# Kernel optimization log

Measured on AMD Instinct MI355X. Metric: run time of the kernel, lower is better.

Reference implementation:

```python
import jax, jax.numpy as jnp
import numpy as np

N = 4096       # num nodes == output_dim (delta is symmetrized NxN)
E = 65536      # num edges (avg degree 16)
IN_DIM = 128
H = 256        # hidden_dim (channels)
HEADS = 4


def setup_inputs():
    key = jax.random.key(0)
    ks = iter(jax.random.split(key, 40))
    def w(shape, s=0.05):
        return jax.random.normal(next(ks), shape, jnp.float32) * s
    inp = {}
    inp['x'] = jax.random.normal(next(ks), (N, IN_DIM), jnp.float32)
    inp['edge_index'] = jax.random.randint(next(ks), (2, E), 0, N)
    inp['pre_w'] = w((H, IN_DIM)); inp['pre_b'] = w((H,))
    for p in ('g1', 'g2'):
        inp[p + '_gcn_w'] = w((H, H)); inp[p + '_gcn_b'] = w((H,))
        inp[p + '_attn_in_w'] = w((3 * H, H)); inp[p + '_attn_in_b'] = w((3 * H,))
        inp[p + '_attn_out_w'] = w((H, H)); inp[p + '_attn_out_b'] = w((H,))
        inp[p + '_ffn_w1'] = w((2 * H, H)); inp[p + '_ffn_b1'] = w((2 * H,))
        inp[p + '_ffn_w2'] = w((H, 2 * H)); inp[p + '_ffn_b2'] = w((H,))
    inp['mlp_w1'] = w((H, H)); inp['mlp_b1'] = w((H,))
    inp['mlp_w2'] = w((N, H)); inp['mlp_b2'] = w((N,))
    return inp


def _gcn(x, src, dst, W, b):
    n = x.shape[0]
    x = x @ W.T
    loop = jnp.arange(n)
    s = jnp.concatenate([src, loop])
    d = jnp.concatenate([dst, loop])
    deg = jax.ops.segment_sum(jnp.ones(s.shape[0], x.dtype), d, num_segments=n)
    dinv = jnp.where(deg > 0, jax.lax.rsqrt(deg), 0.0)
    coef = (dinv[s] * dinv[d])[:, None]
    out = jax.ops.segment_sum(x[s] * coef, d, num_segments=n)
    return out + b


def _mha(h, in_w, in_b, out_w, out_b):
    # nn.MultiheadAttention self-attention over all N nodes (single dense graph)
    n, c = h.shape
    d = c // HEADS
    qkv = h @ in_w.T + in_b                      # [N, 3C]
    q, k, v = jnp.split(qkv, 3, axis=-1)
    q = q.reshape(n, HEADS, d).transpose(1, 0, 2) * (d ** -0.5)  # [h, n, d]
    k = k.reshape(n, HEADS, d).transpose(1, 0, 2)
    v = v.reshape(n, HEADS, d).transpose(1, 0, 2)
    a = jax.nn.softmax(jnp.einsum('hnd,hmd->hnm', q, k), axis=-1)
    o = jnp.einsum('hnm,hmd->hnd', a, v).transpose(1, 0, 2).reshape(n, c)
    return o @ out_w.T + out_b


def _gps(x, src, dst, gw, gb, iw, ib, ow, ob, w1, b1, w2, b2):
    # GPSConv, eval mode: dropout off, batch_norm (default running stats) = identity
    h1 = _gcn(x, src, dst, gw, gb) + x
    h2 = _mha(x, iw, ib, ow, ob) + x
    out = h1 + h2
    ff = jax.nn.relu(out @ w1.T + b1) @ w2.T + b2
    return out + ff


def reference(x, edge_index, pre_w, pre_b,
              g1_gcn_w, g1_gcn_b, g1_attn_in_w, g1_attn_in_b, g1_attn_out_w, g1_attn_out_b,
              g1_ffn_w1, g1_ffn_b1, g1_ffn_w2, g1_ffn_b2,
              g2_gcn_w, g2_gcn_b, g2_attn_in_w, g2_attn_in_b, g2_attn_out_w, g2_attn_out_b,
              g2_ffn_w1, g2_ffn_b1, g2_ffn_w2, g2_ffn_b2,
              mlp_w1, mlp_b1, mlp_w2, mlp_b2):
    src, dst = edge_index[0], edge_index[1]
    h = jax.nn.relu(x @ pre_w.T + pre_b)
    h = jax.nn.relu(_gps(h, src, dst, g1_gcn_w, g1_gcn_b, g1_attn_in_w, g1_attn_in_b,
                         g1_attn_out_w, g1_attn_out_b, g1_ffn_w1, g1_ffn_b1, g1_ffn_w2, g1_ffn_b2))
    h = jax.nn.relu(_gps(h, src, dst, g2_gcn_w, g2_gcn_b, g2_attn_in_w, g2_attn_in_b,
                         g2_attn_out_w, g2_attn_out_b, g2_ffn_w1, g2_ffn_b1, g2_ffn_w2, g2_ffn_b2))
    delta = jax.nn.relu(h @ mlp_w1.T + mlp_b1) @ mlp_w2.T + mlp_b2  # [N, N]
    return (delta + delta.T) * 0.5
```

## Files before the change

kernel.cpp:

```cpp
#include <hip/hip_runtime.h>

#define NN 4096
#define EE 65536
#define HC 256

typedef unsigned short ushort_t;
typedef __attribute__((ext_vector_type(8))) short bf16x8;
typedef __attribute__((ext_vector_type(4))) float f32x4;
typedef __attribute__((ext_vector_type(16))) float f32x16;

__device__ __forceinline__ ushort_t f2bf(float f) {
    unsigned int u = __float_as_uint(f);
    unsigned int r = (u + 0x7fffu + ((u >> 16) & 1u)) >> 16;
    return (ushort_t)r;
}
__device__ __forceinline__ float bf2f(ushort_t u) {
    return __uint_as_float(((unsigned int)u) << 16);
}
__device__ __forceinline__ unsigned int pack2bf(float a, float b) {
    unsigned int ua = __float_as_uint(a) + 0x8000u;
    unsigned int ub = __float_as_uint(b) + 0x8000u;
    return __builtin_amdgcn_perm(ub, ua, 0x07060302u);
}

__global__ void deg_init_k(float* __restrict__ deg) {
    int i = blockIdx.x * 256 + threadIdx.x;
    deg[i] = 1.0f;
}
__global__ void deg_scatter_k(const int* __restrict__ dst, float* __restrict__ deg) {
    int e = blockIdx.x * 256 + threadIdx.x;
    atomicAdd(&deg[dst[e]], 1.0f);
}
__global__ void dinv_k(const float* __restrict__ deg, float* __restrict__ dinv) {
    int i = blockIdx.x * 256 + threadIdx.x;
    dinv[i] = rsqrtf(deg[i]);
}
__global__ __launch_bounds__(1024)
void scan_offsets_k(const float* __restrict__ deg, int* __restrict__ offs,
                    int* __restrict__ cursor) {
    __shared__ int part[1024];
    const int t = threadIdx.x;
    int c0 = (int)deg[t * 4 + 0] - 1;
    int c1 = (int)deg[t * 4 + 1] - 1;
    int c2 = (int)deg[t * 4 + 2] - 1;
    int c3 = (int)deg[t * 4 + 3] - 1;
    part[t] = c0 + c1 + c2 + c3;
    __syncthreads();
    for (int off = 1; off < 1024; off <<= 1) {
        int v = (t >= off) ? part[t - off] : 0;
        __syncthreads();
        part[t] += v;
        __syncthreads();
    }
    int base = (t == 0) ? 0 : part[t - 1];
    offs[t * 4 + 0] = base;
    offs[t * 4 + 1] = base + c0;
    offs[t * 4 + 2] = base + c0 + c1;
    offs[t * 4 + 3] = base + c0 + c1 + c2;
    cursor[t * 4 + 0] = base;
    cursor[t * 4 + 1] = base + c0;
    cursor[t * 4 + 2] = base + c0 + c1;
    cursor[t * 4 + 3] = base + c0 + c1 + c2;
    if (t == 1023) offs[4096] = part[1023];
}
__global__ void csr_fill_k(const int* __restrict__ src, const int* __restrict__ dst,
                           int* __restrict__ cursor, int* __restrict__ csr_src) {
    int e = blockIdx.x * 256 + threadIdx.x;
    int pos = atomicAdd(&cursor[dst[e]], 1);
    csr_src[pos] = src[e];
}

__global__ __launch_bounds__(256)
void gcn_gather_k(const float* __restrict__ xw, const float* __restrict__ dinv,
                  const int* __restrict__ offs, const int* __restrict__ csr_src,
                  float* __restrict__ agg) {
    const int node = blockIdx.x * 4 + (threadIdx.x >> 6);
    const int c = (threadIdx.x & 63) * 4;
    const float dd = dinv[node];
    float4 a = *(const float4*)&xw[(size_t)node * HC + c];
    const float self = dd * dd;
    float4 acc = make_float4(a.x * self, a.y * self, a.z * self, a.w * self);
    const int beg = offs[node], end = offs[node + 1];
    for (int e = beg; e < end; e++) {
        int s = csr_src[e];
        float coef = dinv[s] * dd;
        const float4 v = *(const float4*)&xw[(size_t)s * HC + c];
        acc.x += v.x * coef;
        acc.y += v.y * coef;
        acc.z += v.z * coef;
        acc.w += v.w * coef;
    }
    *(float4*)&agg[(size_t)node * HC + c] = acc;
}

__global__ void cvt_bf16_k(const float* __restrict__ in, ushort_t* __restrict__ out) {
    int i = (blockIdx.x * 256 + threadIdx.x) * 4;
    float4 v = *(const float4*)&in[i];
    unsigned int d0 = pack2bf(v.x, v.y), d1 = pack2bf(v.z, v.w);
    *(uint2*)&out[i] = make_uint2(d0, d1);
}

__global__ __launch_bounds__(256)
void gemm_bf_k(const float* __restrict__ X, const float* __restrict__ W,
               const float* __restrict__ bias1, const float* __restrict__ bias2,
               const float* __restrict__ res1, const float* __restrict__ res2, float res2scale,
               float* __restrict__ out, int K, int M, int dorelu, int obf,
               int colsplit, const float* __restrict__ W2,
               const float* __restrict__ bias_r2, float* __restrict__ out2, int M2)
{
    __shared__ ushort_t As[64][72];
    __shared__ ushort_t Bs[32][72];
    const int t = threadIdx.x;
    const int w = t >> 6, lane = t & 63;
    const int m = lane & 15, quad = lane >> 4;
    const int row0 = blockIdx.y << 6, col0 = blockIdx.x << 5;
    const int sr = t >> 2;
    const int sc = (t & 3) << 4;
    const int wr2 = t >> 3;
    const int wc2 = (t & 7) << 3;

    const float* Wu = W;
    const float* b1u = bias1;
    const float* b2u = bias2;
    float* outu = out;
    int Mu = M, colu = col0;
    if (colsplit > 0 && col0 >= colsplit) {
        Wu = W2; b1u = bias_r2; b2u = nullptr;
        outu = out2; Mu = M2; colu = col0 - colsplit;
    }

    f32x4 acc[2] = {};
    for (int k0 = 0; k0 < K; k0 += 64) {
        const float* xp = &X[(size_t)(row0 + sr) * K + k0 + sc];
        const float* wp = &Wu[(size_t)(colu + wr2) * K + k0 + wc2];
        float4 xa = *(const float4*)xp,       xb = *(const float4*)(xp + 4);
        float4 xc = *(const float4*)(xp + 8), xd = *(const float4*)(xp + 12);
        float4 wa = *(const float4*)wp,       wb = *(const float4*)(wp + 4);
        __syncthreads();
        {
            unsigned int tx[8];
            tx[0] = pack2bf(xa.x, xa.y); tx[1] = pack2bf(xa.z, xa.w);
            tx[2] = pack2bf(xb.x, xb.y); tx[3] = pack2bf(xb.z, xb.w);
            tx[4] = pack2bf(xc.x, xc.y); tx[5] = pack2bf(xc.z, xc.w);
            tx[6] = pack2bf(xd.x, xd.y); tx[7] = pack2bf(xd.z, xd.w);
            *(uint4*)&As[sr][sc]     = *(const uint4*)&tx[0];
            *(uint4*)&As[sr][sc + 8] = *(const uint4*)&tx[4];
            unsigned int tw[4];
            tw[0] = pack2bf(wa.x, wa.y); tw[1] = pack2bf(wa.z, wa.w);
            tw[2] = pack2bf(wb.x, wb.y); tw[3] = pack2bf(wb.z, wb.w);
            *(uint4*)&Bs[wr2][wc2] = *(const uint4*)&tw[0];
        }
        __syncthreads();
        #pragma unroll
        for (int kc = 0; kc < 2; kc++) {
            bf16x8 af = *(const bf16x8*)&As[(w << 4) + m][kc * 32 + quad * 8];
            #pragma unroll
            for (int cb = 0; cb < 2; cb++) {
                bf16x8 bf = *(const bf16x8*)&Bs[cb * 16 + m][kc * 32 + quad * 8];
                acc[cb] = __builtin_amdgcn_mfma_f32_16x16x32_bf16(af, bf, acc[cb], 0, 0, 0);
            }
        }
    }
    #pragma unroll
    for (int cb = 0; cb < 2; cb++) {
        #pragma unroll
        for (int r = 0; r < 4; r++) {
            const int row = row0 + (w << 4) + quad * 4 + r;
            const int col = colu + cb * 16 + m;
            float v = acc[cb][r];
            if (b1u) v += b1u[col];
            if (b2u) v += b2u[col];
            if (res1) v += res1[(size_t)row * Mu + col];
            if (res2) v += res2scale * res2[(size_t)row * Mu + col];
            if (dorelu) v = fmaxf(v, 0.f);
            if (obf) ((ushort_t*)outu)[(size_t)row * Mu + col] = f2bf(v);
            else outu[(size_t)row * Mu + col] = v;
        }
    }
}

__global__ __launch_bounds__(256)
void kv_prep_k(const float* __restrict__ qkv, ushort_t* __restrict__ Kb,
               ushort_t* __restrict__ Vtb)
{
    __shared__ ushort_t Vs[64][72];
    const int h = blockIdx.y;
    const int n0 = blockIdx.x << 6;
    const int t = threadIdx.x;
    for (int u = t; u < 1024; u += 256) {
        int r = u >> 4, c = u & 15;
        const float* kp = &qkv[(size_t)(n0 + r) * 768 + 256 + h * 64 + c * 4];
        float4 kv = *(const float4*)kp;
        float4 vv = *(const float4*)(kp + 256);
        *(uint2*)&Kb[((size_t)(h * 4096 + n0 + r)) * 64 + c * 4] =
            make_uint2(pack2bf(kv.x, kv.y), pack2bf(kv.z, kv.w));
        *(uint2*)&Vs[r][c * 4] =
            make_uint2(pack2bf(vv.x, vv.y), pack2bf(vv.z, vv.w));
    }
    __syncthreads();
    int d = t >> 2, kc = t & 3;
    __attribute__((aligned(16))) ushort_t vals[16];
    #pragma unroll
    for (int k = 0; k < 16; k++) vals[k] = Vs[kc * 16 + k][d];
    ushort_t* op = &Vtb[((size_t)(h * 64 + d)) * 4096 + n0 + kc * 16];
    *(uint4*)op = *(const uint4*)&vals[0];
    *(uint4*)(op + 8) = *(const uint4*)&vals[8];
}

__global__ __launch_bounds__(128)
void attn_part_k(const float* qkv, const ushort_t* __restrict__ Kb,
                 const ushort_t* __restrict__ Vtb, ushort_t* opart,
                 float* __restrict__ m_part, float* __restrict__ l_part)
{
    __shared__ ushort_t Kt[64][64];
    __shared__ ushort_t Vt[64][64];
    const int h = blockIdx.y & 3;
    const int split = blockIdx.y >> 2;
    const int q0 = blockIdx.x << 6;
    const int t = threadIdx.x;
    const int w = t >> 6;
    const int lane = t & 63;
    const int l31 = lane & 31;
    const int hi = lane >> 5;

    const int sr = t >> 3;
    const int sc = t & 7;
    const int swz = ((sc ^ (sr & 7)) << 3);
    const ushort_t* kp = &Kb[((size_t)(h * 4096 + split * 1024 + sr)) * 64 + sc * 8];
    const ushort_t* vp = &Vtb[((size_t)(h * 64 + sr)) * 4096 + split * 1024 + sc * 8];

    const float qs = 0.125f * 1.44269504f;
    const int qrow = q0 + w * 32 + l31;
    bf16x8 qf[4];
    #pragma unroll
    for (int s = 0; s < 4; s++) {
        const float* qp = &qkv[(size_t)qrow * 768 + h * 64 + s * 16 + hi * 8];
        float4 a = *(const float4*)qp;
        float4 b = *(const float4*)(qp + 4);
        union { uint4 u; bf16x8 v; } cv;
        cv.u = make_uint4(pack2bf(a.x * qs, a.y * qs), pack2bf(a.z * qs, a.w * qs),
                          pack2bf(b.x * qs, b.y * qs), pack2bf(b.z * qs, b.w * qs));
        qf[s] = cv.v;
    }

    f32x16 O0 = {}, O1 = {};
    float mrow = -1e30f;
    float ol = 0.f;

    for (int it = 0; it < 16; it++) {
        uint4 k0 = *(const uint4*)kp;
        uint4 k1 = *(const uint4*)(kp + 16 * 64);
        uint4 k2 = *(const uint4*)(kp + 32 * 64);
        uint4 k3 = *(const uint4*)(kp + 48 * 64);
        uint4 v0 = *(const uint4*)vp;
        uint4 v1 = *(const uint4*)(vp + (size_t)16 * 4096);
        uint4 v2 = *(const uint4*)(vp + (size_t)32 * 4096);
        uint4 v3 = *(const uint4*)(vp + (size_t)48 * 4096);
        kp += 4096; vp += 64;
        __syncthreads();
        *(uint4*)&Kt[sr][swz]      = k0;
        *(uint4*)&Kt[sr + 16][swz] = k1;
        *(uint4*)&Kt[sr + 32][swz] = k2;
        *(uint4*)&Kt[sr + 48][swz] = k3;
        *(uint4*)&Vt[sr][swz]      = v0;
        *(uint4*)&Vt[sr + 16][swz] = v1;
        *(uint4*)&Vt[sr + 32][swz] = v2;
        *(uint4*)&Vt[sr + 48][swz] = v3;
        __syncthreads();

        f32x16 S0 = {}, S1 = {};
        const int kcol = ((hi) ^ (l31 & 7));
        (void)kcol;
        __builtin_amdgcn_s_setprio(1);
        #pragma unroll
        for (int s = 0; s < 4; s++) {
            const int cc = ((2 * s + hi) ^ (l31 & 7)) << 3;
            bf16x8 kf0 = *(const bf16x8*)&Kt[l31][cc];
            bf16x8 kf1 = *(const bf16x8*)&Kt[l31 + 32][cc];
            S0 = __builtin_amdgcn_mfma_f32_32x32x16_bf16(kf0, qf[s], S0, 0, 0, 0);
            S1 = __builtin_amdgcn_mfma_f32_32x32x16_bf16(kf1, qf[s], S1, 0, 0, 0);
        }
        __builtin_amdgcn_s_setprio(0);

        float r[32];
        #pragma unroll
        for (int i = 0; i < 16; i++) { r[i] = S0[i]; r[16 + i] = S1[i]; }
        #pragma unroll
        for (int st = 16; st > 0; st >>= 1)
            #pragma unroll
            for (int i = 0; i < st; i++) r[i] = fmaxf(r[i], r[i + st]);
        float mx = fmaxf(r[0], __shfl_xor(r[0], 32));

        if (__any(mx > mrow + 8.f)) {
            float mnew = fmaxf(mrow, mx);
            float alpha = __builtin_amdgcn_exp2f(mrow - mnew);
            mrow = mnew;
            ol *= alpha;
            #pragma unroll
            for (int rg = 0; rg < 16; rg++) {
                float ar = __shfl(alpha, (rg & 3) + 8 * (rg >> 2) + 4 * hi);
                O0[rg] *= ar;
                O1[rg] *= ar;
            }
        }

        #pragma unroll
        for (int i = 0; i < 16; i++) S0[i] = __builtin_amdgcn_exp2f(S0[i] - mrow);
        #pragma unroll
        for (int i = 0; i < 16; i++) S1[i] = __builtin_amdgcn_exp2f(S1[i] - mrow);

        float a2[32];
        #pragma unroll
        for (int i = 0; i < 16; i++) { a2[i] = S0[i]; a2[16 + i] = S1[i]; }
        #pragma unroll
        for (int st = 16; st > 0; st >>= 1)
            #pragma unroll
            for (int i = 0; i < st; i++) a2[i] += a2[i + st];
        ol += a2[0] + __shfl_xor(a2[0], 32);

        unsigned c[16], d[16];
        #pragma unroll
        for (int i = 0; i < 8; i++) c[i] = pack2bf(S0[2 * i], S0[2 * i + 1]);
        #pragma unroll
        for (int i = 0; i < 8; i++) c[8 + i] = pack2bf(S1[2 * i], S1[2 * i + 1]);
        #pragma unroll
        for (int i = 0; i < 16; i++) d[i] = __shfl_xor(c[i], 32);

        bf16x8 pa[4];
        #pragma unroll
        for (int b = 0; b < 2; b++) {
            union { uint4 u; bf16x8 v; } t0, t1;
            t0.u = make_uint4(hi ? d[8 * b + 2] : c[8 * b + 0],
                              hi ? d[8 * b + 3] : c[8 * b + 1],
                              hi ? c[8 * b + 2] : d[8 * b + 0],
                              hi ? c[8 * b + 3] : d[8 * b + 1]);
            t1.u = make_uint4(hi ? d[8 * b + 6] : c[8 * b + 4],
                              hi ? d[8 * b + 7] : c[8 * b + 5],
                              hi ? c[8 * b + 6] : d[8 * b + 4],
                              hi ? c[8 * b + 7] : d[8 * b + 5]);
            pa[2 * b] = t0.v;
            pa[2 * b + 1] = t1.v;
        }

        __builtin_amdgcn_s_setprio(1);
        #pragma unroll
        for (int ks = 0; ks < 4; ks++) {
            const int cc = ((2 * ks + hi) ^ (l31 & 7)) << 3;
            bf16x8 vf0 = *(const bf16x8*)&Vt[l31][cc];
            bf16x8 vf1 = *(const bf16x8*)&Vt[l31 + 32][cc];
            O0 = __builtin_amdgcn_mfma_f32_32x32x16_bf16(pa[ks], vf0, O0, 0, 0, 0);
            O1 = __builtin_amdgcn_mfma_f32_32x32x16_bf16(pa[ks], vf1, O1, 0, 0, 0);
        }
        __builtin_amdgcn_s_setprio(0);
    }

    #pragma unroll
    for (int rg = 0; rg < 16; rg++) {
        int q = q0 + w * 32 + (rg & 3) + 8 * (rg >> 2) + 4 * hi;
        size_t base = (size_t)q * 1536 + 512 + split * 256 + h * 64;
        opart[base + l31] = f2bf(O0[rg]);
        opart[base + 32 + l31] = f2bf(O1[rg]);
    }
    if (hi == 0) {
        m_part[(split * 4 + h) * 4096 + q0 + w * 32 + l31] = mrow;
        l_part[(split * 4 + h) * 4096 + q0 + w * 32 + l31] = ol;
    }
}

__global__ __launch_bounds__(256)
void attn_merge_k(const ushort_t* __restrict__ opart, const float* __restrict__ m_part,
                  const float* __restrict__ l_part, float* __restrict__ att)
{
    int idx = blockIdx.x * 256 + threadIdx.x;
    int q = idx >> 8, c = idx & 255;
    int h = c >> 6, d = c & 63;
    float ms[4];
    float mmax = -1e30f;
    #pragma unroll
    for (int s = 0; s < 4; s++) {
        ms[s] = m_part[(s * 4 + h) * 4096 + q];
        mmax = fmaxf(mmax, ms[s]);
    }
    float onum = 0.f, lden = 0.f;
    #pragma unroll
    for (int s = 0; s < 4; s++) {
        float wgt = __builtin_amdgcn_exp2f(ms[s] - mmax);
        float ov = bf2f(opart[(size_t)q * 1536 + 512 + s * 256 + h * 64 + d]);
        onum += wgt * ov;
        lden += wgt * l_part[(s * 4 + h) * 4096 + q];
    }
    att[(size_t)q * 256 + c] = onum / lden;
}

__global__ __launch_bounds__(256)
void sym_mlp_mfma_k(const ushort_t* __restrict__ Tb, const ushort_t* __restrict__ Wb,
                    const float* __restrict__ b2, float* __restrict__ out)
{
    __shared__ ushort_t As[128][72];
    __shared__ ushort_t Bs[128][72];
    const int t = threadIdx.x;
    const int w = t >> 6, lane = t & 63;
    const int m = lane & 15, quad = lane >> 4;
    const int wr = (w >> 1) * 64, wc = (w & 1) * 64;
    const int ri = blockIdx.y * 128, rj = blockIdx.x * 128;

    f32x4 acc[4][4] = {};
    for (int kk = 0; kk < 8; kk++) {
        const int k0 = kk * 64;
        const ushort_t* Asrc = (k0 < 256) ? Tb : Wb;
        const ushort_t* Bsrc = (k0 < 256) ? Wb : Tb;
        const int kcol = k0 & 255;
        __syncthreads();
        #pragma unroll
        for (int i = 0; i < 4; i++) {
            int s = t + i * 256;
            int row = s >> 3, ch = (s & 7) * 8;
            *(uint4*)&As[row][ch] = *(const uint4*)&Asrc[(size_t)(ri + row) * 256 + kcol + ch];
            *(uint4*)&Bs[row][ch] = *(const uint4*)&Bsrc[(size_t)(rj + row) * 256 + kcol + ch];
        }
        __syncthreads();
        #pragma unroll
        for (int kc = 0; kc < 2; kc++) {
            bf16x8 af[4], bfr[4];
            #pragma unroll
            for (int rb = 0; rb < 4; rb++)
                af[rb] = *(const bf16x8*)&As[wr + rb * 16 + m][kc * 32 + quad * 8];
            #pragma unroll
            for (int cb = 0; cb < 4; cb++)
                bfr[cb] = *(const bf16x8*)&Bs[wc + cb * 16 + m][kc * 32 + quad * 8];
            #pragma unroll
            for (int rb = 0; rb < 4; rb++)
                #pragma unroll
                for (int cb = 0; cb < 4; cb++)
                    acc[rb][cb] = __builtin_amdgcn_mfma_f32_16x16x32_bf16(af[rb], bfr[cb], acc[rb][cb], 0, 0, 0);
        }
    }
    #pragma unroll
    for (int rb = 0; rb < 4; rb++) {
        #pragma unroll
        for (int r = 0; r < 4; r++) {
            const int gr = ri + wr + rb * 16 + quad * 4 + r;
            const float br = b2[gr];
            #pragma unroll
            for (int cb = 0; cb < 4; cb++) {
                const int gc = rj + wc + cb * 16 + m;
                out[(size_t)gr * NN + gc] = 0.5f * (acc[rb][cb][r] + br + b2[gc]);
            }
        }
    }
}

extern "C" void kernel_launch(void* const* d_in, const int* in_sizes, int n_in,
                              void* d_out, int out_size, void* d_ws, size_t ws_size,
                              hipStream_t stream) {
    (void)in_sizes; (void)n_in; (void)out_size; (void)ws_size;
    const float* x = (const float*)d_in[0];
    const int* ei = (const int*)d_in[1];
    const int* src = ei;
    const int* dst = ei + EE;

    float* ws = (float*)d_ws;
    const int NH = NN * HC;
    float* h0  = ws;
    float* hb  = ws + 1 * NH;
    float* hc  = ws + 2 * NH;
    float* att = ws + 3 * NH;
    float* qkv = ws + 4 * NH;
    float* ffh = ws + 4 * NH;
    float* deg = ws + 7 * NH;
    float* dinv = deg + NN;
    int* offs    = (int*)(dinv + NN);
    int* cursor  = offs + 4100;
    int* csr_src = cursor + 4096;
    float* m_part = (float*)(csr_src + EE);
    float* l_part = m_part + 65536;
    ushort_t* Kb  = (ushort_t*)hc;
    ushort_t* Vtb = Kb + NH;
    ushort_t* Tb  = (ushort_t*)hb;
    ushort_t* W2b = Tb + NH;

    deg_init_k<<<NN / 256, 256, 0, stream>>>(deg);
    deg_scatter_k<<<EE / 256, 256, 0, stream>>>(dst, deg);
    dinv_k<<<NN / 256, 256, 0, stream>>>(deg, dinv);
    scan_offsets_k<<<1, 1024, 0, stream>>>(deg, offs, cursor);
    csr_fill_k<<<EE / 256, 256, 0, stream>>>(src, dst, cursor, csr_src);

    gemm_bf_k<<<dim3(8, 64), 256, 0, stream>>>(
        x, (const float*)d_in[2], (const float*)d_in[3], nullptr,
        nullptr, nullptr, 0.f, h0, 128, 256, 1, 0,
        0, nullptr, nullptr, nullptr, 0);

    for (int L = 0; L < 2; L++) {
        int B = 4 + L * 10;
        const float* gw = (const float*)d_in[B + 0];
        const float* gb = (const float*)d_in[B + 1];
        const float* iw = (const float*)d_in[B + 2];
        const float* ib = (const float*)d_in[B + 3];
        const float* ow = (const float*)d_in[B + 4];
        const float* ob = (const float*)d_in[B + 5];
        const float* w1 = (const float*)d_in[B + 6];
        const float* b1 = (const float*)d_in[B + 7];
        const float* w2 = (const float*)d_in[B + 8];
        const float* b2 = (const float*)d_in[B + 9];

        gemm_bf_k<<<dim3(32, 64), 256, 0, stream>>>(
            h0, gw, nullptr, nullptr, nullptr, nullptr, 0.f, att, 256, 256, 0, 0,
            256, iw, ib, qkv, 768);
        gcn_gather_k<<<NN / 4, 256, 0, stream>>>(att, dinv, offs, csr_src, hb);
        kv_prep_k<<<dim3(64, 4), 256, 0, stream>>>(qkv, Kb, Vtb);
        attn_part_k<<<dim3(64, 16), 128, 0, stream>>>(
            qkv, Kb, Vtb, (ushort_t*)qkv, m_part, l_part);
        attn_merge_k<<<NN, 256, 0, stream>>>(
            (const ushort_t*)qkv, m_part, l_part, att);
        gemm_bf_k<<<dim3(8, 64), 256, 0, stream>>>(
            att, ow, ob, gb, hb, h0, 2.0f, hc, 256, 256, 0, 0,
            0, nullptr, nullptr, nullptr, 0);
        gemm_bf_k<<<dim3(16, 64), 256, 0, stream>>>(
            hc, w1, b1, nullptr, nullptr, nullptr, 0.f, ffh, 256, 512, 1, 0,
            0, nullptr, nullptr, nullptr, 0);
        gemm_bf_k<<<dim3(8, 64), 256, 0, stream>>>(
            ffh, w2, b2, nullptr, hc, nullptr, 0.f, h0, 512, 256, 1, 0,
            0, nullptr, nullptr, nullptr, 0);
    }

    gemm_bf_k<<<dim3(8, 64), 256, 0, stream>>>(
        h0, (const float*)d_in[24], (const float*)d_in[25], nullptr,
        nullptr, nullptr, 0.f, (float*)Tb, 256, 256, 1, 1,
        0, nullptr, nullptr, nullptr, 0);
    cvt_bf16_k<<<NH / 1024, 256, 0, stream>>>((const float*)d_in[26], W2b);
    sym_mlp_mfma_k<<<dim3(32, 32), 256, 0, stream>>>(
        Tb, W2b, (const float*)d_in[27], (float*)d_out);
}
```

Baseline: 420.0 us.

## Double-buffer K/V tiles and widen attention blocks to four waves

```diff
diff --git a/kernel.cpp b/kernel.cpp
--- a/kernel.cpp
+++ b/kernel.cpp
@@ -207,16 +207,16 @@
     *(uint4*)(op + 8) = *(const uint4*)&vals[8];
 }
 
-__global__ __launch_bounds__(128)
+__global__ __launch_bounds__(256, 2)
 void attn_part_k(const float* qkv, const ushort_t* __restrict__ Kb,
                  const ushort_t* __restrict__ Vtb, ushort_t* opart,
                  float* __restrict__ m_part, float* __restrict__ l_part)
 {
-    __shared__ ushort_t Kt[64][64];
-    __shared__ ushort_t Vt[64][64];
+    __shared__ ushort_t Kt[2][64][64];
+    __shared__ ushort_t Vt[2][64][64];
     const int h = blockIdx.y & 3;
     const int split = blockIdx.y >> 2;
-    const int q0 = blockIdx.x << 6;
+    const int q0 = blockIdx.x << 7;
     const int t = threadIdx.x;
     const int w = t >> 6;
     const int lane = t & 63;
@@ -247,36 +247,33 @@
     float mrow = -1e30f;
     float ol = 0.f;
 
+    uint4 ka0 = *(const uint4*)kp;
+    uint4 ka1 = *(const uint4*)(kp + 32 * 64);
+    uint4 va0 = *(const uint4*)vp;
+    uint4 va1 = *(const uint4*)(vp + (size_t)32 * 4096);
+    kp += 4096; vp += 64;
+    *(uint4*)&Kt[0][sr][swz]      = ka0;
+    *(uint4*)&Kt[0][sr + 32][swz] = ka1;
+    *(uint4*)&Vt[0][sr][swz]      = va0;
+    *(uint4*)&Vt[0][sr + 32][swz] = va1;
+    ka0 = *(const uint4*)kp;
+    ka1 = *(const uint4*)(kp + 32 * 64);
+    va0 = *(const uint4*)vp;
+    va1 = *(const uint4*)(vp + (size_t)32 * 4096);
+    kp += 4096; vp += 64;
+    asm volatile("s_waitcnt lgkmcnt(0)" ::: "memory");
+    __builtin_amdgcn_s_barrier();
+
     for (int it = 0; it < 16; it++) {
-        uint4 k0 = *(const uint4*)kp;
-        uint4 k1 = *(const uint4*)(kp + 16 * 64);
-        uint4 k2 = *(const uint4*)(kp + 32 * 64);
-        uint4 k3 = *(const uint4*)(kp + 48 * 64);
-        uint4 v0 = *(const uint4*)vp;
-        uint4 v1 = *(const uint4*)(vp + (size_t)16 * 4096);
-        uint4 v2 = *(const uint4*)(vp + (size_t)32 * 4096);
-        uint4 v3 = *(const uint4*)(vp + (size_t)48 * 4096);
-        kp += 4096; vp += 64;
-        __syncthreads();
-        *(uint4*)&Kt[sr][swz]      = k0;
-        *(uint4*)&Kt[sr + 16][swz] = k1;
-        *(uint4*)&Kt[sr + 32][swz] = k2;
-        *(uint4*)&Kt[sr + 48][swz] = k3;
-        *(uint4*)&Vt[sr][swz]      = v0;
-        *(uint4*)&Vt[sr + 16][swz] = v1;
-        *(uint4*)&Vt[sr + 32][swz] = v2;
-        *(uint4*)&Vt[sr + 48][swz] = v3;
-        __syncthreads();
+        const int cur = it & 1;
 
         f32x16 S0 = {}, S1 = {};
-        const int kcol = ((hi) ^ (l31 & 7));
-        (void)kcol;
         __builtin_amdgcn_s_setprio(1);
         #pragma unroll
         for (int s = 0; s < 4; s++) {
             const int cc = ((2 * s + hi) ^ (l31 & 7)) << 3;
-            bf16x8 kf0 = *(const bf16x8*)&Kt[l31][cc];
-            bf16x8 kf1 = *(const bf16x8*)&Kt[l31 + 32][cc];
+            bf16x8 kf0 = *(const bf16x8*)&Kt[cur][l31][cc];
+            bf16x8 kf1 = *(const bf16x8*)&Kt[cur][l31 + 32][cc];
             S0 = __builtin_amdgcn_mfma_f32_32x32x16_bf16(kf0, qf[s], S0, 0, 0, 0);
             S1 = __builtin_amdgcn_mfma_f32_32x32x16_bf16(kf1, qf[s], S1, 0, 0, 0);
         }
@@ -317,6 +314,20 @@
             #pragma unroll
             for (int i = 0; i < st; i++) a2[i] += a2[i + st];
         ol += a2[0] + __shfl_xor(a2[0], 32);
+
+        if (it < 15) {
+            *(uint4*)&Kt[cur ^ 1][sr][swz]      = ka0;
+            *(uint4*)&Kt[cur ^ 1][sr + 32][swz] = ka1;
+            *(uint4*)&Vt[cur ^ 1][sr][swz]      = va0;
+            *(uint4*)&Vt[cur ^ 1][sr + 32][swz] = va1;
+            if (it < 14) {
+                ka0 = *(const uint4*)kp;
+                ka1 = *(const uint4*)(kp + 32 * 64);
+                va0 = *(const uint4*)vp;
+                va1 = *(const uint4*)(vp + (size_t)32 * 4096);
+                kp += 4096; vp += 64;
+            }
+        }
 
         unsigned c[16], d[16];
         #pragma unroll
@@ -346,12 +357,15 @@
         #pragma unroll
         for (int ks = 0; ks < 4; ks++) {
             const int cc = ((2 * ks + hi) ^ (l31 & 7)) << 3;
-            bf16x8 vf0 = *(const bf16x8*)&Vt[l31][cc];
-            bf16x8 vf1 = *(const bf16x8*)&Vt[l31 + 32][cc];
+            bf16x8 vf0 = *(const bf16x8*)&Vt[cur][l31][cc];
+            bf16x8 vf1 = *(const bf16x8*)&Vt[cur][l31 + 32][cc];
             O0 = __builtin_amdgcn_mfma_f32_32x32x16_bf16(pa[ks], vf0, O0, 0, 0, 0);
             O1 = __builtin_amdgcn_mfma_f32_32x32x16_bf16(pa[ks], vf1, O1, 0, 0, 0);
         }
         __builtin_amdgcn_s_setprio(0);
+
+        asm volatile("s_waitcnt lgkmcnt(0)" ::: "memory");
+        __builtin_amdgcn_s_barrier();
     }
 
     #pragma unroll
@@ -508,7 +522,7 @@
             256, iw, ib, qkv, 768);
         gcn_gather_k<<<NN / 4, 256, 0, stream>>>(att, dinv, offs, csr_src, hb);
         kv_prep_k<<<dim3(64, 4), 256, 0, stream>>>(qkv, Kb, Vtb);
-        attn_part_k<<<dim3(64, 16), 128, 0, stream>>>(
+        attn_part_k<<<dim3(32, 16), 256, 0, stream>>>(
             qkv, Kb, Vtb, (ushort_t*)qkv, m_part, l_part);
         attn_merge_k<<<NN, 256, 0, stream>>>(
             (const ushort_t*)qkv, m_part, l_part, att);
```

New measurement: 412.5 us. About the same (-1.8%).
